# Optimization experiments

Hardware: AMD Instinct MI355X
Metric: run time of the kernel (lower is better)

The kernel has to match this reference:

```python
import jax, jax.numpy as jnp
import numpy as np

B, C_I, C_O, K, H, W = 8, 64, 64, 3, 256, 256
GROUPS = 16  # int(c_o / min(4, c_o)) = 64/4
EPS = 1e-5
PAD = K  # pad_x = pad_y = k + (bc-1) with bc_x=bc_y=1, k=3


def _conv(x, w):
    # x: (B, C_i, h, w), w: (C_o, C_i, K, K), valid conv, stride 1
    return jax.lax.conv_general_dilated(
        x, w, window_strides=(1, 1), padding='VALID',
        dimension_numbers=('NCHW', 'OIHW', 'NCHW'))


def setup_inputs() -> dict:
    key = jax.random.key(0)
    ks = jax.random.split(key, 10)
    s = 1.0 / np.sqrt(C_I * K * K)  # torch Conv2d default init bound
    wshape = (C_O, C_I, K, K)
    names = ['w_int', 'w_tl', 'w_tr', 'w_bl', 'w_br', 'w_top', 'w_bot', 'w_left', 'w_right']
    d = {'x': jax.random.normal(ks[0], (B, C_I, H, W), dtype=jnp.float32)}
    for i, n in enumerate(names):
        d[n] = jax.random.uniform(ks[i + 1], wshape, jnp.float32, -s, s)
    d['bias'] = jnp.zeros((1, C_O, 1, 1), jnp.float32)   # learnable_bias (init zeros)
    d['gamma'] = jnp.ones((C_O,), jnp.float32)           # GroupNorm weight
    d['beta'] = jnp.zeros((C_O,), jnp.float32)           # GroupNorm bias
    return d


def reference(x, w_int, w_tl, w_tr, w_bl, w_br, w_top, w_bot, w_left, w_right, bias, gamma, beta):
    p = PAD
    # corners -> (B,C,1,1)
    tl = _conv(x[:, :, :p, :p], w_tl)
    tr = _conv(x[:, :, :p, -p:], w_tr)
    bl = _conv(x[:, :, -p:, :p], w_bl)
    br = _conv(x[:, :, -p:, -p:], w_br)
    # edges -> (B,C,1,W-2) / (B,C,H-2,1)
    top = _conv(x[:, :, :p, :], w_top)
    bot = _conv(x[:, :, -p:, :], w_bot)
    left = _conv(x[:, :, :, :p], w_left)
    right = _conv(x[:, :, :, -p:], w_right)
    # interior -> (B,C,H-2,W-2)
    mid = _conv(x, w_int)
    mid = jnp.concatenate([left, mid, right], axis=3)       # (B,C,H-2,W)
    top_row = jnp.concatenate([tl, top, tr], axis=3)        # (B,C,1,W)
    bot_row = jnp.concatenate([bl, bot, br], axis=3)        # (B,C,1,W)
    # NOTE: original code puts the 'bottom' conv output first along dim 2
    y = jnp.concatenate([bot_row, mid, top_row], axis=2) + bias  # (B,C,H,W)
    # GroupNorm(16, 64)
    yg = y.reshape(B, GROUPS, -1)
    mu = jnp.mean(yg, axis=2, keepdims=True)
    var = jnp.var(yg, axis=2, keepdims=True)
    yn = ((yg - mu) * jax.lax.rsqrt(var + EPS)).reshape(B, C_O, H, W)
    yn = yn * gamma[None, :, None, None] + beta[None, :, None, None]
    # SELU activation; dropout(rate=0) is identity
    return jax.nn.selu(yn)
```

## Files before the change

kernel.cpp:

```cpp
#include <hip/hip_runtime.h>

#define B_ 8
#define CI 64
#define CO 64
#define H_ 256
#define W_ 256
#define EPS_ 1e-5f

#define SELU_SCALE 1.0507009873554805f
#define SELU_SA    1.7580993408473766f

typedef __attribute__((ext_vector_type(8))) short short8;
typedef __attribute__((ext_vector_type(4))) float f32x4;
typedef unsigned int u32;

__device__ __forceinline__ unsigned short f2bf(float f) {
    unsigned int u = __float_as_uint(f);
    u = (u + 0x7fffu + ((u >> 16) & 1u)) >> 16;
    return (unsigned short)u;
}
__device__ __forceinline__ float bf2f(unsigned short h) {
    return __uint_as_float(((unsigned)h) << 16);
}
__device__ __forceinline__ float selu_f(float u) {
    return (u > 0.f) ? SELU_SCALE * u : SELU_SA * (__expf(u) - 1.f);
}
__device__ __forceinline__ void gload_lds16(const void* g, void* l) {
    __builtin_amdgcn_global_load_lds(
        (const __attribute__((address_space(1))) u32*)g,
        (__attribute__((address_space(3))) u32*)l, 16, 0, 0);
}

__global__ __launch_bounds__(256) void prepass_weights(
    const float* __restrict__ w_int,
    const float* __restrict__ w_bl, const float* __restrict__ w_br,
    const float* __restrict__ w_tl, const float* __restrict__ w_tr,
    const float* __restrict__ w_bot, const float* __restrict__ w_top,
    const float* __restrict__ w_left, const float* __restrict__ w_right,
    unsigned short* __restrict__ wpre, float* __restrict__ wedge)
{
    const int blk = blockIdx.x, t = threadIdx.x;
    if (blk < 72) {
        const int wid = blk / 9, pos = blk % 9;
        const float* src = (wid == 0) ? w_bl : (wid == 1) ? w_br
                         : (wid == 2) ? w_tl : (wid == 3) ? w_tr
                         : (wid == 4) ? w_bot : (wid == 5) ? w_top
                         : (wid == 6) ? w_left : w_right;
        float* dst = wedge + (size_t)blk * 4096;
        for (int k = 0; k < 16; ++k) {
            const int lin = k * 256 + t;
            const int c4  = lin >> 8;
            const int co  = (lin >> 2) & 63;
            const int j   = lin & 3;
            const int ci  = c4 * 4 + j;
            dst[lin] = src[(co * 64 + ci) * 9 + pos];
        }
    } else {
        const int pos = blk - 72;
        for (int k = 0; k < 16; ++k) {
            const int lin = k * 256 + t;
            const int co = lin >> 6, cip = lin & 63;
            const int ci = cip ^ ((co & 7) << 3);
            wpre[pos * 4096 + lin] = f2bf(w_int[(co * 64 + ci) * 9 + pos]);
        }
    }
}

__global__ __launch_bounds__(256) void prepass_x(
    const float* __restrict__ x, unsigned short* __restrict__ xpre)
{
    __shared__ unsigned short ls[256 * 72];
    const int row = blockIdx.x, b = blockIdx.y;
    const int t = threadIdx.x;
    const int colq = t >> 2;
    const float* xb = x + ((size_t)(b * 64) * 256 + row) * 256;

    for (int sp = 0; sp < 4; ++sp) {
        const int cibase = sp * 16 + (t & 3) * 4;
        float4 v[4];
#pragma unroll
        for (int e = 0; e < 4; ++e)
            v[e] = *(const float4*)(xb + (size_t)(cibase + e) * 65536 + colq * 4);
#pragma unroll
        for (int jj = 0; jj < 4; ++jj) {
            const int col = colq * 4 + jj;
            const int sw  = (col & 7) << 3;
            ushort4 pk;
            pk.x = f2bf((&v[0].x)[jj]);
            pk.y = f2bf((&v[1].x)[jj]);
            pk.z = f2bf((&v[2].x)[jj]);
            pk.w = f2bf((&v[3].x)[jj]);
            *(ushort4*)&ls[col * 72 + (cibase ^ sw)] = pk;
        }
    }
    __syncthreads();
    unsigned short* xp = xpre + ((size_t)(b * 256 + row)) * 256 * 64;
    for (int q = 0; q < 8; ++q) {
        const int lin = q * 256 + t;
        const int col = lin >> 3, k = lin & 7;
        *(uint4*)(xp + col * 64 + k * 8) = *(const uint4*)&ls[col * 72 + k * 8];
    }
}

__global__ __launch_bounds__(512, 4) void conv_mfma(
    const unsigned short* __restrict__ xpre, const unsigned short* __restrict__ wpre,
    const float* __restrict__ bias, unsigned short* __restrict__ ybf,
    float* __restrict__ part)
{
    __shared__ unsigned short xs[10 * 40 * 64];
    __shared__ unsigned short wl3[3][4096];
    __shared__ float sred[8][16][2];
    const int t = threadIdx.x, w = t >> 6, lane = t & 63;
    const int b = blockIdx.z, r0 = blockIdx.y * 8, c0 = blockIdx.x * 32;

    for (int L = w; L < 50; L += 8) {
        const int j = L / 5, i = L % 5;
        int rr = r0 - 1 + j; rr = rr < 0 ? 0 : (rr > 255 ? 255 : rr);
        int col = c0 - 2 + i * 8 + (lane >> 3);
        col = col < 0 ? 0 : (col > 255 ? 255 : col);
        const char* src = (const char*)xpre +
            ((size_t)((b * 256 + rr) * 256 + col)) * 128 + (lane & 7) * 16;
        gload_lds16(src, (char*)xs + j * 5120 + i * 1024);
    }
    gload_lds16((const char*)wpre + 0 * 8192 + w * 1024 + lane * 16,
                (char*)wl3[0] + w * 1024);
    gload_lds16((const char*)wpre + 1 * 8192 + w * 1024 + lane * 16,
                (char*)wl3[1] + w * 1024);

    const int l15 = lane & 15, lg = lane >> 4;
    const int sw15 = (l15 & 7) << 3;

    int jb[3];
#pragma unroll
    for (int kr = 0; kr < 3; ++kr) jb[kr] = (w + kr) * 5120;
    int offb[3][2][2];
#pragma unroll
    for (int kc = 0; kc < 3; ++kc)
#pragma unroll
        for (int n = 0; n < 2; ++n) {
            const int s = n * 16 + l15 + kc + 1;
#pragma unroll
            for (int ks = 0; ks < 2; ++ks) {
                const int cib = ks * 32 + lg * 8;
                offb[kc][n][ks] = s * 128 + ((cib ^ (((s + 6) & 7) << 3)) << 1);
            }
        }
    int afo[2][4];
#pragma unroll
    for (int ks = 0; ks < 2; ++ks)
#pragma unroll
        for (int m = 0; m < 4; ++m) {
            const int cib = ks * 32 + lg * 8;
            afo[ks][m] = (m * 16 + l15) * 128 + ((cib ^ sw15) << 1);
        }

    f32x4 acc[4][2];
#pragma unroll
    for (int m = 0; m < 4; ++m)
#pragma unroll
        for (int n = 0; n < 2; ++n)
            acc[m][n] = (f32x4){0.f, 0.f, 0.f, 0.f};

#pragma unroll
    for (int pos = 0; pos < 9; ++pos) {
        if (pos < 8) asm volatile("s_waitcnt vmcnt(1)" ::: "memory");
        else         asm volatile("s_waitcnt vmcnt(0)" ::: "memory");
        __builtin_amdgcn_s_barrier();
        __builtin_amdgcn_sched_barrier(0);
        if (pos + 2 <= 8)
            gload_lds16((const char*)wpre + (pos + 2) * 8192 + w * 1024 + lane * 16,
                        (char*)wl3[(pos + 2) % 3] + w * 1024);
        const int kr = pos / 3, kc = pos % 3;
        const char* wbuf = (const char*)wl3[pos % 3];
#pragma unroll
        for (int ks = 0; ks < 2; ++ks) {
            short8 bf[2], af[4];
#pragma unroll
            for (int n = 0; n < 2; ++n)
                bf[n] = *(const short8*)((const char*)xs + jb[kr] + offb[kc][n][ks]);
#pragma unroll
            for (int m = 0; m < 4; ++m)
                af[m] = *(const short8*)(wbuf + afo[ks][m]);
            __builtin_amdgcn_s_setprio(1);
#pragma unroll
            for (int m = 0; m < 4; ++m)
#pragma unroll
                for (int n = 0; n < 2; ++n)
                    acc[m][n] = __builtin_amdgcn_mfma_f32_16x16x32_bf16(
                        af[m], bf[n], acc[m][n], 0, 0, 0);
            __builtin_amdgcn_s_setprio(0);
        }
    }

    const int r = r0 + w;
    const bool rmask = (r != 0) && (r != 255);
    float s4[4] = {0.f, 0.f, 0.f, 0.f}, q4[4] = {0.f, 0.f, 0.f, 0.f};
#pragma unroll
    for (int m = 0; m < 4; ++m)
#pragma unroll
        for (int n = 0; n < 2; ++n) {
            const int c = c0 + n * 16 + l15;
            const bool pmask = rmask && (c != 0) && (c != 255);
#pragma unroll
            for (int reg = 0; reg < 4; ++reg) {
                const int co = m * 16 + lg * 4 + reg;
                const float v = acc[m][n][reg] + bias[co];
                ybf[(((size_t)b * 64 + co) * 256 + r) * 256 + c] = f2bf(v);
                if (pmask) { s4[m] += v; q4[m] += v * v; }
            }
        }
#pragma unroll
    for (int off = 1; off < 16; off <<= 1)
#pragma unroll
        for (int m = 0; m < 4; ++m) {
            s4[m] += __shfl_xor(s4[m], off);
            q4[m] += __shfl_xor(q4[m], off);
        }
    if (l15 == 0) {
#pragma unroll
        for (int m = 0; m < 4; ++m) {
            sred[w][m * 4 + lg][0] = s4[m];
            sred[w][m * 4 + lg][1] = q4[m];
        }
    }
    __syncthreads();
    if (t < 32) {
        const int g = t & 15, sel = t >> 4;
        float v = 0.f;
#pragma unroll
        for (int ww = 0; ww < 8; ++ww) v += sred[ww][g][sel];
        const int slot = blockIdx.y * 8 + blockIdx.x;
        part[((size_t)(b * 512 + slot) * 16 + g) * 2 + sel] = v;
    }
}

__global__ __launch_bounds__(256) void conv_edge2(
    const unsigned short* __restrict__ xpre, const float* __restrict__ wedge,
    const float* __restrict__ bias, unsigned short* __restrict__ ybf,
    float* __restrict__ part)
{
    __shared__ float xl[4][9][64];
    __shared__ float ered[4][16][2];
    const int b = blockIdx.x, edge = blockIdx.y, seg = blockIdx.z;
    const int t = threadIdx.x, p = t >> 6, lane = t & 63;

    for (int unit = t; unit < 288; unit += 256) {
        const int chunk = unit >> 3, sub = unit & 7;
        const int pp = chunk / 9, rem = chunk % 9, kr = rem / 3, kc = rem % 3;
        int e = seg * 4 + pp;
        if (edge >= 2 && e > 253) e = 253;
        int row, colb;
        if (edge == 0)      { row = 253 + kr; colb = (e == 0) ? 0 : ((e == 255) ? 253 : (e - 1)); }
        else if (edge == 1) { row = kr;       colb = (e == 0) ? 0 : ((e == 255) ? 253 : (e - 1)); }
        else if (edge == 2) { row = e + kr;   colb = 0; }
        else                { row = e + kr;   colb = 253; }
        const int col = colb + kc;
        const uint4 v = *(const uint4*)(xpre +
            ((size_t)((b * 256 + row) * 256 + col)) * 64 + sub * 8);
        const int ci0 = (sub ^ (col & 7)) * 8;
        float* dst = &xl[pp][kr * 3 + kc][ci0];
        const unsigned short* hv = (const unsigned short*)&v;
#pragma unroll
        for (int j = 0; j < 8; ++j) dst[j] = bf2f(hv[j]);
    }
    __syncthreads();

    int e = seg * 4 + p;
    const bool active = (edge < 2) || (e <= 253);
    if (edge >= 2 && e > 253) e = 253;
    int wid, r_out, c_out;
    if (edge == 0)      { wid = (e == 0) ? 0 : ((e == 255) ? 1 : 4); r_out = 0;   c_out = e; }
    else if (edge == 1) { wid = (e == 0) ? 2 : ((e == 255) ? 3 : 5); r_out = 255; c_out = e; }
    else if (edge == 2) { wid = 6; r_out = e + 1; c_out = 0; }
    else                { wid = 7; r_out = e + 1; c_out = 255; }

    const int co = lane;
    float acc = 0.f;
    const float* wbase = wedge + (size_t)wid * 36864;
#pragma unroll
    for (int pos = 0; pos < 9; ++pos) {
        const float* wp = wbase + pos * 4096 + lane * 4;
        const float* xp = &xl[p][pos][0];
#pragma unroll
        for (int c4 = 0; c4 < 16; ++c4) {
            const float4 wv = *(const float4*)(wp + c4 * 256);
            const float4 xv = *(const float4*)(xp + c4 * 4);
            acc = fmaf(wv.x, xv.x, acc); acc = fmaf(wv.y, xv.y, acc);
            acc = fmaf(wv.z, xv.z, acc); acc = fmaf(wv.w, xv.w, acc);
        }
    }
    const float v = acc + bias[co];
    if (active) ybf[(((size_t)b * 64 + co) * 256 + r_out) * 256 + c_out] = f2bf(v);
    float s = active ? v : 0.f, q = active ? v * v : 0.f;
    s += __shfl_xor(s, 1); q += __shfl_xor(q, 1);
    s += __shfl_xor(s, 2); q += __shfl_xor(q, 2);
    if ((lane & 3) == 0) { ered[p][co >> 2][0] = s; ered[p][co >> 2][1] = q; }
    __syncthreads();
    if (t < 32) {
        const int g = t & 15, sel = t >> 4;
        const float r = ered[0][g][sel] + ered[1][g][sel] +
                        ered[2][g][sel] + ered[3][g][sel];
        const int slot = 256 + (edge * 64 + seg);
        part[((size_t)(b * 512 + slot) * 16 + g) * 2 + sel] = r;
    }
}

__global__ __launch_bounds__(256) void stats_reduce(
    const float* __restrict__ part, float* __restrict__ mv)
{
    __shared__ float sred[16][16][2];
    const int b = blockIdx.x, t = threadIdx.x;
    const int g = t & 15, chunk = t >> 4;
    float s = 0.f, q = 0.f;
    for (int k = 0; k < 32; ++k) {
        const int slot = chunk * 32 + k;
        const size_t base = ((size_t)(b * 512 + slot) * 16 + g) * 2;
        s += part[base]; q += part[base + 1];
    }
    sred[chunk][g][0] = s; sred[chunk][g][1] = q;
    __syncthreads();
    if (t < 16) {
        float S = 0.f, Q = 0.f;
#pragma unroll
        for (int c = 0; c < 16; ++c) { S += sred[c][t][0]; Q += sred[c][t][1]; }
        const float inv_n = 1.0f / (4.0f * 65536.0f);
        const float mean = S * inv_n;
        const float var  = Q * inv_n - mean * mean;
        mv[(b * 16 + t) * 2]     = mean;
        mv[(b * 16 + t) * 2 + 1] = rsqrtf(var + EPS_);
    }
}

__global__ __launch_bounds__(256) void norm_bf(
    const unsigned short* __restrict__ ybf, float* __restrict__ out,
    const float* __restrict__ mv,
    const float* __restrict__ gamma, const float* __restrict__ beta)
{
    const size_t tt = (size_t)blockIdx.x * 256 + threadIdx.x;
    const size_t e = tt * 8;
    const int b  = (int)(e >> 22);
    const int ch = (int)((e >> 16) & 63);
    const int g  = ch >> 2;
    const float mean = mv[(b * 16 + g) * 2];
    const float rstd = mv[(b * 16 + g) * 2 + 1];
    const float ga = gamma[ch] * rstd;
    const float be = beta[ch] - mean * ga;

    const uint4 v = *(const uint4*)(ybf + e);
    float f[8];
    f[0] = __uint_as_float(v.x << 16); f[1] = __uint_as_float(v.x & 0xffff0000u);
    f[2] = __uint_as_float(v.y << 16); f[3] = __uint_as_float(v.y & 0xffff0000u);
    f[4] = __uint_as_float(v.z << 16); f[5] = __uint_as_float(v.z & 0xffff0000u);
    f[6] = __uint_as_float(v.w << 16); f[7] = __uint_as_float(v.w & 0xffff0000u);
    float4 o0, o1;
    o0.x = selu_f(f[0] * ga + be); o0.y = selu_f(f[1] * ga + be);
    o0.z = selu_f(f[2] * ga + be); o0.w = selu_f(f[3] * ga + be);
    o1.x = selu_f(f[4] * ga + be); o1.y = selu_f(f[5] * ga + be);
    o1.z = selu_f(f[6] * ga + be); o1.w = selu_f(f[7] * ga + be);
    *(float4*)(out + e)     = o0;
    *(float4*)(out + e + 4) = o1;
}

__global__ __launch_bounds__(256) void conv_main(
    const float* __restrict__ x, const float* __restrict__ w,
    const float* __restrict__ bias, float* __restrict__ y)
{
    const int c = threadIdx.x;
    const int r = blockIdx.x;
    const int b = blockIdx.y;
    const int rr = (r == 0) ? (H_ - 3) : ((r == H_ - 1) ? 0 : (r - 1));
    const int cc = min(max(c - 1, 0), W_ - 3);
    float acc[CO];
#pragma unroll
    for (int co = 0; co < CO; ++co) acc[co] = 0.f;
    const float* xb = x + (size_t)b * CI * H_ * W_;
    for (int ci = 0; ci < CI; ++ci) {
        const float* xp = xb + ((size_t)ci * H_ + rr) * W_ + cc;
        float xv[9];
#pragma unroll
        for (int kr = 0; kr < 3; ++kr)
#pragma unroll
            for (int kc = 0; kc < 3; ++kc)
                xv[kr * 3 + kc] = xp[kr * W_ + kc];
        const float* wci = w + ci * 9;
#pragma unroll
        for (int co = 0; co < CO; ++co) {
            const float* wp = wci + co * (CI * 9);
            float a = acc[co];
#pragma unroll
            for (int k = 0; k < 9; ++k) a = fmaf(xv[k], wp[k], a);
            acc[co] = a;
        }
    }
#pragma unroll
    for (int co = 0; co < CO; ++co)
        y[(((size_t)b * CO + co) * H_ + r) * W_ + c] = acc[co] + bias[co];
}

__global__ __launch_bounds__(256) void conv_edge(
    const float* __restrict__ x,
    const float* __restrict__ w_bot, const float* __restrict__ w_top,
    const float* __restrict__ w_left, const float* __restrict__ w_right,
    const float* __restrict__ bias, float* __restrict__ y)
{
    const int b     = blockIdx.x;
    const int edge  = blockIdx.y;
    const int seg   = blockIdx.z;
    const int el    = threadIdx.x & 63;
    const int chunk = threadIdx.x >> 6;
    const int e     = seg * 64 + el;
    const bool active = (e < 254);
    const int ec    = active ? e : 253;
    const float* w = (edge == 0) ? w_bot : (edge == 1) ? w_top
                   : (edge == 2) ? w_left : w_right;
    int r_out, c_out, rr, cc;
    if (edge == 0)      { r_out = 0;      c_out = 1 + ec; rr = H_ - 3; cc = ec; }
    else if (edge == 1) { r_out = H_ - 1; c_out = 1 + ec; rr = 0;      cc = ec; }
    else if (edge == 2) { r_out = 1 + ec; c_out = 0;      rr = ec;     cc = 0; }
    else                { r_out = 1 + ec; c_out = W_ - 1; rr = ec;     cc = W_ - 3; }
    float acc[CO];
#pragma unroll
    for (int co = 0; co < CO; ++co) acc[co] = 0.f;
    const float* xb = x + (size_t)b * CI * H_ * W_;
    const int ci0 = chunk * 16;
    for (int ci = ci0; ci < ci0 + 16; ++ci) {
        const float* xp = xb + ((size_t)ci * H_ + rr) * W_ + cc;
        float xv[9];
#pragma unroll
        for (int kr = 0; kr < 3; ++kr)
#pragma unroll
            for (int kc = 0; kc < 3; ++kc)
                xv[kr * 3 + kc] = xp[kr * W_ + kc];
#pragma unroll
        for (int co = 0; co < CO; ++co) {
            const float* wp = w + co * (CI * 9) + ci * 9;
            float a = acc[co];
#pragma unroll
            for (int k = 0; k < 9; ++k) a = fmaf(xv[k], wp[k], a);
            acc[co] = a;
        }
    }
    __shared__ float lds[64][65];
    for (int s = 0; s < 4; ++s) {
        if (chunk == s) {
            if (s == 0) {
#pragma unroll
                for (int co = 0; co < CO; ++co) lds[el][co] = acc[co];
            } else {
#pragma unroll
                for (int co = 0; co < CO; ++co) lds[el][co] += acc[co];
            }
        }
        __syncthreads();
    }
    if (chunk == 0 && active) {
#pragma unroll
        for (int co = 0; co < CO; ++co)
            y[(((size_t)b * CO + co) * H_ + r_out) * W_ + c_out] = lds[el][co] + bias[co];
    }
}

__global__ __launch_bounds__(256) void conv_corner(
    const float* __restrict__ x,
    const float* __restrict__ w_bl, const float* __restrict__ w_br,
    const float* __restrict__ w_tl, const float* __restrict__ w_tr,
    const float* __restrict__ bias, float* __restrict__ y)
{
    const int b      = blockIdx.x;
    const int corner = threadIdx.x >> 6;
    const int co     = threadIdx.x & 63;
    const float* w = (corner == 0) ? w_bl : (corner == 1) ? w_br
                   : (corner == 2) ? w_tl : w_tr;
    const int rr    = (corner < 2) ? (H_ - 3) : 0;
    const int cc    = (corner & 1) ? (W_ - 3) : 0;
    const int r_out = (corner < 2) ? 0 : (H_ - 1);
    const int c_out = (corner & 1) ? (W_ - 1) : 0;
    const float* xb = x + (size_t)b * CI * H_ * W_;
    float a = 0.f;
    for (int ci = 0; ci < CI; ++ci) {
        const float* xp = xb + ((size_t)ci * H_ + rr) * W_ + cc;
        const float* wp = w + ((size_t)co * CI + ci) * 9;
#pragma unroll
        for (int kr = 0; kr < 3; ++kr)
#pragma unroll
            for (int kc = 0; kc < 3; ++kc)
                a = fmaf(xp[kr * W_ + kc], wp[kr * 3 + kc], a);
    }
    y[(((size_t)b * CO + co) * H_ + r_out) * W_ + c_out] = a + bias[co];
}

__global__ __launch_bounds__(256) void stats_kernel(
    const float* __restrict__ y, float* __restrict__ ws)
{
    const int bid   = blockIdx.x;
    const int chunk = bid & 3;
    const int g     = (bid >> 2) & 15;
    const int b     = bid >> 6;
    const float* p  = y + ((size_t)(b * 64 + g * 4 + chunk)) * (H_ * W_);
    float s = 0.f, q = 0.f;
    for (int i = threadIdx.x; i < (H_ * W_ / 4); i += 256) {
        float4 v = reinterpret_cast<const float4*>(p)[i];
        s += v.x + v.y + v.z + v.w;
        q += v.x * v.x + v.y * v.y + v.z * v.z + v.w * v.w;
    }
#pragma unroll
    for (int off = 32; off; off >>= 1) {
        s += __shfl_down(s, off);
        q += __shfl_down(q, off);
    }
    __shared__ float red[8];
    const int wid = threadIdx.x >> 6;
    if ((threadIdx.x & 63) == 0) { red[wid * 2] = s; red[wid * 2 + 1] = q; }
    __syncthreads();
    if (threadIdx.x == 0) {
        ws[bid * 2]     = red[0] + red[2] + red[4] + red[6];
        ws[bid * 2 + 1] = red[1] + red[3] + red[5] + red[7];
    }
}

__global__ __launch_bounds__(256) void norm_stats(
    float* __restrict__ y, const float* __restrict__ st,
    const float* __restrict__ gamma, const float* __restrict__ beta)
{
    const size_t t = (size_t)blockIdx.x * 256 + threadIdx.x;
    const size_t e = t * 4;
    const int b  = (int)(e >> 22);
    const int ch = (int)((e >> 16) & 63);
    const int g  = ch >> 2;
    const int sb = ((b * 16 + g) * 4) * 2;
    const float S = st[sb] + st[sb + 2] + st[sb + 4] + st[sb + 6];
    const float Q = st[sb + 1] + st[sb + 3] + st[sb + 5] + st[sb + 7];
    const float inv_n = 1.0f / (4.0f * H_ * W_);
    const float mean  = S * inv_n;
    const float var   = Q * inv_n - mean * mean;
    const float rstd  = rsqrtf(var + EPS_);
    const float ga = gamma[ch] * rstd;
    const float be = beta[ch] - mean * ga;
    float4 v = reinterpret_cast<float4*>(y)[t];
    float u;
    u = v.x * ga + be; v.x = selu_f(u);
    u = v.y * ga + be; v.y = selu_f(u);
    u = v.z * ga + be; v.z = selu_f(u);
    u = v.w * ga + be; v.w = selu_f(u);
    reinterpret_cast<float4*>(y)[t] = v;
}

extern "C" void kernel_launch(void* const* d_in, const int* in_sizes, int n_in,
                              void* d_out, int out_size, void* d_ws, size_t ws_size,
                              hipStream_t stream) {
    const float* x       = (const float*)d_in[0];
    const float* w_int   = (const float*)d_in[1];
    const float* w_tl    = (const float*)d_in[2];
    const float* w_tr    = (const float*)d_in[3];
    const float* w_bl    = (const float*)d_in[4];
    const float* w_br    = (const float*)d_in[5];
    const float* w_top   = (const float*)d_in[6];
    const float* w_bot   = (const float*)d_in[7];
    const float* w_left  = (const float*)d_in[8];
    const float* w_right = (const float*)d_in[9];
    const float* bias    = (const float*)d_in[10];
    const float* gamma   = (const float*)d_in[11];
    const float* beta    = (const float*)d_in[12];

    float* out = (float*)d_out;

    const size_t XPRE  = 67108864ull;
    const size_t YBF   = 67108864ull;
    const size_t WPRE  = 73728ull;
    const size_t WEDGE = 1179648ull;
    const size_t PART  = 524288ull;
    const size_t MV    = 1024ull;
    const size_t NEED  = XPRE + YBF + WPRE + WEDGE + PART + MV;

    if (ws_size >= NEED) {
        unsigned short* xpre = (unsigned short*)d_ws;
        unsigned short* ybf  = (unsigned short*)((char*)d_ws + XPRE);
        unsigned short* wpre = (unsigned short*)((char*)d_ws + XPRE + YBF);
        float* wedge = (float*)((char*)d_ws + XPRE + YBF + WPRE);
        float* part  = (float*)((char*)d_ws + XPRE + YBF + WPRE + WEDGE);
        float* mv    = (float*)((char*)d_ws + XPRE + YBF + WPRE + WEDGE + PART);

        prepass_weights<<<dim3(81), 256, 0, stream>>>(
            w_int, w_bl, w_br, w_tl, w_tr, w_bot, w_top, w_left, w_right, wpre, wedge);
        prepass_x<<<dim3(256, 8), 256, 0, stream>>>(x, xpre);
        conv_mfma<<<dim3(8, 32, 8), 512, 0, stream>>>(xpre, wpre, bias, ybf, part);
        conv_edge2<<<dim3(8, 4, 64), 256, 0, stream>>>(xpre, wedge, bias, ybf, part);
        stats_reduce<<<dim3(8), 256, 0, stream>>>(part, mv);
        norm_bf<<<dim3(16384), 256, 0, stream>>>(ybf, out, mv, gamma, beta);
    } else {
        float* stats = (float*)d_ws;
        conv_main<<<dim3(H_, B_), 256, 0, stream>>>(x, w_int, bias, out);
        conv_edge<<<dim3(B_, 4, 4), 256, 0, stream>>>(x, w_bot, w_top, w_left, w_right, bias, out);
        conv_corner<<<dim3(B_), 256, 0, stream>>>(x, w_bl, w_br, w_tl, w_tr, bias, out);
        stats_kernel<<<dim3(512), 256, 0, stream>>>(out, stats);
        norm_stats<<<dim3(32768), 256, 0, stream>>>(out, stats, gamma, beta);
    }
}
```

Baseline: 178.8 us.

## Compute two output rows per wave in conv_mfma with 256-thread blocks

The MFMA conv block shrinks from 8 waves to 4, and each wave now computes two output rows with two accumulator sets. The weight A-fragments loaded from LDS are reused across both rows, which halves weight LDS reads per MFMA, and the staging loads and wait counts are adjusted to match. In exchange, register pressure rises because accumulators double, there are fewer waves per block to hide latency, and the launch bounds change the occupancy target.

```diff
diff --git a/kernel.cpp b/kernel.cpp
--- a/kernel.cpp
+++ b/kernel.cpp
@@ -102,18 +102,18 @@
     }
 }
 
-__global__ __launch_bounds__(512, 4) void conv_mfma(
+__global__ __launch_bounds__(256, 2) void conv_mfma(
     const unsigned short* __restrict__ xpre, const unsigned short* __restrict__ wpre,
     const float* __restrict__ bias, unsigned short* __restrict__ ybf,
     float* __restrict__ part)
 {
     __shared__ unsigned short xs[10 * 40 * 64];
     __shared__ unsigned short wl3[3][4096];
-    __shared__ float sred[8][16][2];
+    __shared__ float sred[4][16][2];
     const int t = threadIdx.x, w = t >> 6, lane = t & 63;
     const int b = blockIdx.z, r0 = blockIdx.y * 8, c0 = blockIdx.x * 32;
 
-    for (int L = w; L < 50; L += 8) {
+    for (int L = w; L < 50; L += 4) {
         const int j = L / 5, i = L % 5;
         int rr = r0 - 1 + j; rr = rr < 0 ? 0 : (rr > 255 ? 255 : rr);
         int col = c0 - 2 + i * 8 + (lane >> 3);
@@ -122,17 +122,24 @@
             ((size_t)((b * 256 + rr) * 256 + col)) * 128 + (lane & 7) * 16;
         gload_lds16(src, (char*)xs + j * 5120 + i * 1024);
     }
-    gload_lds16((const char*)wpre + 0 * 8192 + w * 1024 + lane * 16,
-                (char*)wl3[0] + w * 1024);
-    gload_lds16((const char*)wpre + 1 * 8192 + w * 1024 + lane * 16,
-                (char*)wl3[1] + w * 1024);
+#pragma unroll
+    for (int c = 0; c < 2; ++c)
+        gload_lds16((const char*)wpre + 0 * 8192 + (w * 2 + c) * 1024 + lane * 16,
+                    (char*)wl3[0] + (w * 2 + c) * 1024);
+#pragma unroll
+    for (int c = 0; c < 2; ++c)
+        gload_lds16((const char*)wpre + 1 * 8192 + (w * 2 + c) * 1024 + lane * 16,
+                    (char*)wl3[1] + (w * 2 + c) * 1024);
 
     const int l15 = lane & 15, lg = lane >> 4;
     const int sw15 = (l15 & 7) << 3;
 
-    int jb[3];
-#pragma unroll
-    for (int kr = 0; kr < 3; ++kr) jb[kr] = (w + kr) * 5120;
+    int jbA[3], jbB[3];
+#pragma unroll
+    for (int kr = 0; kr < 3; ++kr) {
+        jbA[kr] = (2 * w + kr) * 5120;
+        jbB[kr] = (2 * w + 1 + kr) * 5120;
+    }
     int offb[3][2][2];
 #pragma unroll
     for (int kc = 0; kc < 3; ++kc)
@@ -154,30 +161,37 @@
             afo[ks][m] = (m * 16 + l15) * 128 + ((cib ^ sw15) << 1);
         }
 
-    f32x4 acc[4][2];
+    f32x4 accA[4][2], accB[4][2];
 #pragma unroll
     for (int m = 0; m < 4; ++m)
 #pragma unroll
-        for (int n = 0; n < 2; ++n)
-            acc[m][n] = (f32x4){0.f, 0.f, 0.f, 0.f};
+        for (int n = 0; n < 2; ++n) {
+            accA[m][n] = (f32x4){0.f, 0.f, 0.f, 0.f};
+            accB[m][n] = (f32x4){0.f, 0.f, 0.f, 0.f};
+        }
 
 #pragma unroll
     for (int pos = 0; pos < 9; ++pos) {
-        if (pos < 8) asm volatile("s_waitcnt vmcnt(1)" ::: "memory");
+        if (pos < 8) asm volatile("s_waitcnt vmcnt(2)" ::: "memory");
         else         asm volatile("s_waitcnt vmcnt(0)" ::: "memory");
         __builtin_amdgcn_s_barrier();
         __builtin_amdgcn_sched_barrier(0);
-        if (pos + 2 <= 8)
-            gload_lds16((const char*)wpre + (pos + 2) * 8192 + w * 1024 + lane * 16,
-                        (char*)wl3[(pos + 2) % 3] + w * 1024);
+        if (pos + 2 <= 8) {
+#pragma unroll
+            for (int c = 0; c < 2; ++c)
+                gload_lds16((const char*)wpre + (pos + 2) * 8192 + (w * 2 + c) * 1024 + lane * 16,
+                            (char*)wl3[(pos + 2) % 3] + (w * 2 + c) * 1024);
+        }
         const int kr = pos / 3, kc = pos % 3;
         const char* wbuf = (const char*)wl3[pos % 3];
 #pragma unroll
         for (int ks = 0; ks < 2; ++ks) {
-            short8 bf[2], af[4];
-#pragma unroll
-            for (int n = 0; n < 2; ++n)
-                bf[n] = *(const short8*)((const char*)xs + jb[kr] + offb[kc][n][ks]);
+            short8 bfA[2], bfB[2], af[4];
+#pragma unroll
+            for (int n = 0; n < 2; ++n) {
+                bfA[n] = *(const short8*)((const char*)xs + jbA[kr] + offb[kc][n][ks]);
+                bfB[n] = *(const short8*)((const char*)xs + jbB[kr] + offb[kc][n][ks]);
+            }
 #pragma unroll
             for (int m = 0; m < 4; ++m)
                 af[m] = *(const short8*)(wbuf + afo[ks][m]);
@@ -185,30 +199,53 @@
 #pragma unroll
             for (int m = 0; m < 4; ++m)
 #pragma unroll
-                for (int n = 0; n < 2; ++n)
-                    acc[m][n] = __builtin_amdgcn_mfma_f32_16x16x32_bf16(
-                        af[m], bf[n], acc[m][n], 0, 0, 0);
+                for (int n = 0; n < 2; ++n) {
+                    accA[m][n] = __builtin_amdgcn_mfma_f32_16x16x32_bf16(
+                        af[m], bfA[n], accA[m][n], 0, 0, 0);
+                    accB[m][n] = __builtin_amdgcn_mfma_f32_16x16x32_bf16(
+                        af[m], bfB[n], accB[m][n], 0, 0, 0);
+                }
             __builtin_amdgcn_s_setprio(0);
         }
     }
 
-    const int r = r0 + w;
-    const bool rmask = (r != 0) && (r != 255);
     float s4[4] = {0.f, 0.f, 0.f, 0.f}, q4[4] = {0.f, 0.f, 0.f, 0.f};
-#pragma unroll
-    for (int m = 0; m < 4; ++m)
-#pragma unroll
-        for (int n = 0; n < 2; ++n) {
-            const int c = c0 + n * 16 + l15;
-            const bool pmask = rmask && (c != 0) && (c != 255);
-#pragma unroll
-            for (int reg = 0; reg < 4; ++reg) {
-                const int co = m * 16 + lg * 4 + reg;
-                const float v = acc[m][n][reg] + bias[co];
-                ybf[(((size_t)b * 64 + co) * 256 + r) * 256 + c] = f2bf(v);
-                if (pmask) { s4[m] += v; q4[m] += v * v; }
+    {
+        const int r = r0 + 2 * w;
+        const bool rmask = (r != 0) && (r != 255);
+#pragma unroll
+        for (int m = 0; m < 4; ++m)
+#pragma unroll
+            for (int n = 0; n < 2; ++n) {
+                const int c = c0 + n * 16 + l15;
+                const bool pmask = rmask && (c != 0) && (c != 255);
+#pragma unroll
+                for (int reg = 0; reg < 4; ++reg) {
+                    const int co = m * 16 + lg * 4 + reg;
+                    const float v = accA[m][n][reg] + bias[co];
+                    ybf[(((size_t)b * 64 + co) * 256 + r) * 256 + c] = f2bf(v);
+                    if (pmask) { s4[m] += v; q4[m] += v * v; }
+                }
             }
-        }
+    }
+    {
+        const int r = r0 + 2 * w + 1;
+        const bool rmask = (r != 0) && (r != 255);
+#pragma unroll
+        for (int m = 0; m < 4; ++m)
+#pragma unroll
+            for (int n = 0; n < 2; ++n) {
+                const int c = c0 + n * 16 + l15;
+                const bool pmask = rmask && (c != 0) && (c != 255);
+#pragma unroll
+                for (int reg = 0; reg < 4; ++reg) {
+                    const int co = m * 16 + lg * 4 + reg;
+                    const float v = accB[m][n][reg] + bias[co];
+                    ybf[(((size_t)b * 64 + co) * 256 + r) * 256 + c] = f2bf(v);
+                    if (pmask) { s4[m] += v; q4[m] += v * v; }
+                }
+            }
+    }
 #pragma unroll
     for (int off = 1; off < 16; off <<= 1)
 #pragma unroll
@@ -228,7 +265,7 @@
         const int g = t & 15, sel = t >> 4;
         float v = 0.f;
 #pragma unroll
-        for (int ww = 0; ww < 8; ++ww) v += sred[ww][g][sel];
+        for (int ww = 0; ww < 4; ++ww) v += sred[ww][g][sel];
         const int slot = blockIdx.y * 8 + blockIdx.x;
         part[((size_t)(b * 512 + slot) * 16 + g) * 2 + sel] = v;
     }
@@ -583,7 +620,7 @@
         prepass_weights<<<dim3(81), 256, 0, stream>>>(
             w_int, w_bl, w_br, w_tl, w_tr, w_bot, w_top, w_left, w_right, wpre, wedge);
         prepass_x<<<dim3(256, 8), 256, 0, stream>>>(x, xpre);
-        conv_mfma<<<dim3(8, 32, 8), 512, 0, stream>>>(xpre, wpre, bias, ybf, part);
+        conv_mfma<<<dim3(8, 32, 8), 256, 0, stream>>>(xpre, wpre, bias, ybf, part);
         conv_edge2<<<dim3(8, 4, 64), 256, 0, stream>>>(xpre, wedge, bias, ybf, part);
         stats_reduce<<<dim3(8), 256, 0, stream>>>(part, mv);
         norm_bf<<<dim3(16384), 256, 0, stream>>>(ybf, out, mv, gamma, beta);
```

Result: no change. 180.1 us (+0.7%).
